# Kernel optimization log

Hardware: AMD Instinct MI355X
Metric: run time of the kernel (lower is better)

Reference implementation:

```python
import jax, jax.numpy as jnp
import numpy as np

B, N, NFEAT, NHID, NHEADS, NBLK = 8, 512, 32, 128, 4, 6


def _lrelu(x):
    return jax.nn.leaky_relu(x, 0.01)


def _layernorm(x, eps=1e-5):
    m = jnp.mean(x, axis=-1, keepdims=True)
    v = jnp.mean((x - m) ** 2, axis=-1, keepdims=True)
    return (x - m) / jnp.sqrt(v + eps)


def _gat(x, W, a, mask, concat):
    # x:[b,n,f]  W:[H,f,o]  a:[H,2o]  mask:[b,n,n] bool
    o = W.shape[-1]
    Wh = jnp.einsum('bnf,hfo->hbno', x, W)
    s1 = jnp.einsum('hbno,ho->hbn', Wh, a[:, :o])   # Wh @ a[:o]
    s2 = jnp.einsum('hbno,ho->hbn', Wh, a[:, o:])   # Wh @ a[o:]
    # rank-1 score: e[i,j] = leakyrelu(s1[i]*s2[j])
    e = _lrelu(s1[:, :, :, None] * s2[:, :, None, :])  # [h,b,n,n]
    e = jnp.where(mask[None], e, jnp.float32(-9e15))
    att = jax.nn.softmax(e, axis=-1)
    att = jnp.where(mask[None], att, jnp.float32(0.0))
    hp = jnp.einsum('hbij,hbjo->hbio', att, Wh)
    return jax.nn.elu(hp) if concat else hp


def _attn_block(x, W, a, rW, rb, mask):
    res = x
    h = _gat(x, W, a, mask, True)                      # [H,b,n,o]
    h = jnp.moveaxis(h, 0, 2).reshape(x.shape[0], x.shape[1], -1)  # concat heads
    h = h @ rW + rb
    if h.shape[-1] == res.shape[-1]:
        h = h + res
    return _layernorm(h)


def _fel(x, f1w1, f1b1, f1w2, f1b2, f2w1, f2b1, f2w2, f2b2, f3w1, f3b1, f3w2, f3b2):
    res = _lrelu(_lrelu(x @ f1w1 + f1b1) @ f1w2 + f1b2)
    h = _lrelu(_lrelu(res @ f2w1 + f2b1) @ f2w2 + f2b2)
    x = _layernorm(h + res)
    res = x
    h = _lrelu(res @ f3w1 + f3b1) @ f3w2 + f3b2
    return _layernorm(h + res)


def setup_inputs() -> dict:
    key = jax.random.key(0)
    ks = iter(jax.random.split(key, 24))
    nrm = lambda shape: jax.random.normal(next(ks), shape, jnp.float32) * 0.05
    inp = {}
    inp['x'] = jax.random.normal(next(ks), (B, N, NFEAT), jnp.float32)
    inp['adj'] = jax.random.randint(next(ks), (B, N, N), 0, 2, jnp.int32)
    inp['layer_id'] = 0
    inp['f1w1'] = nrm((NFEAT, NHID)); inp['f1b1'] = jnp.zeros((NHID,), jnp.float32)
    inp['f1w2'] = nrm((NHID, NHID)); inp['f1b2'] = jnp.zeros((NHID,), jnp.float32)
    inp['f2w1'] = nrm((NHID, 2 * NHID)); inp['f2b1'] = jnp.zeros((2 * NHID,), jnp.float32)
    inp['f2w2'] = nrm((2 * NHID, NHID)); inp['f2b2'] = jnp.zeros((NHID,), jnp.float32)
    inp['f3w1'] = nrm((NHID, 2 * NHID)); inp['f3b1'] = jnp.zeros((2 * NHID,), jnp.float32)
    inp['f3w2'] = nrm((2 * NHID, NHID)); inp['f3b2'] = jnp.zeros((NHID,), jnp.float32)
    inp['att_W'] = nrm((NBLK, NHEADS, NHID, NHID))
    inp['att_a'] = nrm((NBLK, NHEADS, 2 * NHID))
    inp['resh_W'] = nrm((NBLK, NHEADS * NHID, NHID))
    inp['resh_b'] = jnp.zeros((NBLK, NHID), jnp.float32)
    inp['out_W'] = nrm((2, NHID, NHID))
    inp['out_a'] = nrm((2, 2 * NHID))
    inp['proj_W'] = nrm((2 * NHID, 1))
    inp['proj_b'] = jnp.zeros((1,), jnp.float32)
    return inp


def reference(x, adj, layer_id, f1w1, f1b1, f1w2, f1b2, f2w1, f2b1, f2w2, f2b2,
              f3w1, f3b1, f3w2, f3b2, att_W, att_a, resh_W, resh_b, out_W, out_a,
              proj_W, proj_b):
    mask = adj > 0
    mask_t = jnp.transpose(adj, (0, 2, 1)) > 0
    h = _fel(x, f1w1, f1b1, f1w2, f1b2, f2w1, f2b1, f2w2, f2b2, f3w1, f3b1, f3w2, f3b2)
    for i in range(3):
        h = _attn_block(h, att_W[i], att_a[i], resh_W[i], resh_b[i], mask)
    h = _lrelu(_gat(h, out_W[0:1], out_a[0:1], mask, False)[0])
    ht = h
    for i in range(3, 6):
        ht = _attn_block(ht, att_W[i], att_a[i], resh_W[i], resh_b[i], mask_t)
    ht = _lrelu(_gat(ht, out_W[1:2], out_a[1:2], mask_t, False)[0])
    z = jnp.concatenate([h, ht], axis=-1)   # [b,n,2*nhid]
    z = jnp.mean(z, axis=1)                 # sum/length
    return jnp.squeeze(z @ proj_W + proj_b, axis=1)
```

## Files before the change

kernel.cpp:

```cpp
#include <hip/hip_runtime.h>
#include <math.h>

#define B 8
#define N 512
#define D 128
#define H 4
#define TOK (B*N)

typedef __attribute__((ext_vector_type(8))) short bfrag;
typedef __attribute__((ext_vector_type(4))) float facc;
typedef unsigned short u16;
typedef unsigned int u32;
typedef unsigned long long u64;

__device__ __forceinline__ float lrelu(float x){ return x > 0.f ? x : 0.01f*x; }
__device__ __forceinline__ u16 f2bf(float f){
  u32 u = __float_as_uint(f);
  u += 0x7fffu + ((u >> 16) & 1u);
  return (u16)(u >> 16);
}
__device__ __forceinline__ u32 pk2(float a, float b){
  return (u32)f2bf(a) | ((u32)f2bf(b) << 16);
}

#define LS 72
#define ASF 264
#define ASW 136

__global__ void prep_kernel(const int* __restrict__ adj,
    u32* __restrict__ mbits, u32* __restrict__ mtbits,
    float* __restrict__ colsumF, float* __restrict__ colsumT,
    const float* s0, const float* s1_, const float* s2_, const float* s3,
    const float* s4, const float* s5, const float* s6, const float* s7,
    const float* s8,
    u16* d0, u16* d1, u16* d2, u16* d3, u16* d4, u16* d5, u16* d6, u16* d7, u16* d8)
{
  __shared__ int smem[64*65];
  const int tid = threadIdx.x;
  if (blockIdx.x < 512){
    const int tb = blockIdx.x;
    const int b = tb >> 6, i0 = ((tb >> 3) & 7)*64, j0 = (tb & 7)*64;
    #pragma unroll
    for (int i = 0; i < 4; ++i){
      const int r = i*16 + (tid >> 4);
      const int c = (tid & 15)*4;
      int4 v = *(const int4*)&adj[((size_t)b*N + i0 + r)*N + j0 + c];
      smem[r*65 + c]     = v.x; smem[r*65 + c + 1] = v.y;
      smem[r*65 + c + 2] = v.z; smem[r*65 + c + 3] = v.w;
    }
    __syncthreads();
    const int wv = tid >> 6, lane = tid & 63;
    #pragma unroll
    for (int q = 0; q < 16; ++q){
      const int r = wv*16 + q;
      u64 bf_ = __ballot(smem[r*65 + lane] > 0);
      if (lane == 0)
        *(u64*)&mbits[((size_t)b*N + i0 + r)*16 + (j0 >> 5)] = bf_;
      u64 bt_ = __ballot(smem[lane*65 + r] > 0);
      if (lane == 0)
        *(u64*)&mtbits[((size_t)b*N + j0 + r)*16 + (i0 >> 5)] = bt_;
    }
  } else if (blockIdx.x < 1460){
    float* ftile = (float*)smem;
    const int tx = tid & 31, ty = tid >> 5;
    const float* srcs[9] = {s0,s1_,s2_,s3,s4,s5,s6,s7,s8};
    u16* dsts[9] = {d0,d1,d2,d3,d4,d5,d6,d7,d8};
    const int Ks[9] = {32,128,128,256,128,256,128,128,512};
    const int Ns[9] = {128,128,256,128,256,128,128,128,128};
    const int zs[9] = {1,1,1,1,1,1,24,2,6};
    const int job = (int)blockIdx.x - 512;
    int m = 0, base = 0;
    for (; m < 9; ++m){
      int cnt = (Ks[m]>>5)*(Ns[m]>>5)*zs[m];
      if (job < base + cnt) break;
      base += cnt;
    }
    const int rem = job - base;
    const int tn = Ns[m] >> 5;
    const int per = (Ks[m] >> 5)*tn;
    const int z = rem / per, t = rem % per;
    const int k0 = (t / tn)*32, n0 = (t % tn)*32;
    const float* src = srcs[m] + (size_t)z*Ks[m]*Ns[m];
    u16* dst = dsts[m] + (size_t)z*Ks[m]*Ns[m];
    for (int r = ty; r < 32; r += 8)
      ftile[r*33 + tx] = src[(size_t)(k0+r)*Ns[m] + n0 + tx];
    __syncthreads();
    for (int r = ty; r < 32; r += 8)
      dst[(size_t)(n0+r)*Ks[m] + k0 + tx] = f2bf(ftile[tx*33 + r]);
  } else {
    float4 z = {0.f,0.f,0.f,0.f};
    *(float4*)&colsumF[tid*4] = z;
    *(float4*)&colsumT[tid*4] = z;
  }
}

struct BPre { uint4 a,b,c,d; };
__device__ __forceinline__ BPre preB64(const u16* __restrict__ BTn, int ldb, int k0, int tid){
  const int n = tid >> 1, part = tid & 1;
  const u16* wp = BTn + (size_t)n*ldb + k0 + part*32;
  BPre r;
  r.a = *(const uint4*)wp;      r.b = *(const uint4*)(wp+8);
  r.c = *(const uint4*)(wp+16); r.d = *(const uint4*)(wp+24);
  return r;
}
__device__ __forceinline__ void landB64(const BPre& p, u16* Bs, int tid){
  const int n = tid >> 1, part = tid & 1;
  u16* bp = &Bs[n*LS + part*32];
  *(uint4*)bp = p.a; *(uint4*)(bp+8) = p.b; *(uint4*)(bp+16) = p.c; *(uint4*)(bp+24) = p.d;
}
__device__ __forceinline__ void stageB32(const u16* __restrict__ BTn, int ldb,
                                         int k0, u16* Bs, int tid){
  const int n = tid >> 1, part = tid & 1;
  const u16* wp = BTn + (size_t)n*ldb + k0 + part*16;
  uint4 w0 = *(const uint4*)wp, w1 = *(const uint4*)(wp+8);
  *(uint4*)&Bs[n*LS + part*16]     = w0;
  *(uint4*)&Bs[n*LS + part*16 + 8] = w1;
}

__device__ __forceinline__ void mfma64s(const u16* As, int sA, const u16* Bs,
                                        facc acc[4], int r0, int c0, int quad, int l15){
  #pragma unroll
  for (int kk = 0; kk < 2; ++kk){
    bfrag af = *(const bfrag*)&As[(r0 + l15)*sA + kk*32 + quad*8];
    #pragma unroll
    for (int g = 0; g < 4; ++g){
      bfrag bf = *(const bfrag*)&Bs[(c0 + g*16 + l15)*LS + kk*32 + quad*8];
      acc[g] = __builtin_amdgcn_mfma_f32_16x16x32_bf16(af, bf, acc[g], 0,0,0);
    }
  }
}
__device__ __forceinline__ void mfma32s(const u16* As, int sA, const u16* Bs,
                                        facc acc[4], int r0, int c0, int quad, int l15){
  bfrag af = *(const bfrag*)&As[(r0 + l15)*sA + quad*8];
  #pragma unroll
  for (int g = 0; g < 4; ++g){
    bfrag bf = *(const bfrag*)&Bs[(c0 + g*16 + l15)*LS + quad*8];
    acc[g] = __builtin_amdgcn_mfma_f32_16x16x32_bf16(af, bf, acc[g], 0,0,0);
  }
}
__device__ __forceinline__ void mfma64w(const u16* As, const u16* Bs,
                                        facc acc[2][2], int c0,
                                        int quad, int l15){
  #pragma unroll
  for (int kk = 0; kk < 2; ++kk){
    bfrag af0 = *(const bfrag*)&As[(l15)*LS      + kk*32 + quad*8];
    bfrag af1 = *(const bfrag*)&As[(16 + l15)*LS + kk*32 + quad*8];
    #pragma unroll
    for (int f = 0; f < 2; ++f){
      bfrag bf = *(const bfrag*)&Bs[(c0 + f*16 + l15)*LS + kk*32 + quad*8];
      acc[0][f] = __builtin_amdgcn_mfma_f32_16x16x32_bf16(af0, bf, acc[0][f], 0,0,0);
      acc[1][f] = __builtin_amdgcn_mfma_f32_16x16x32_bf16(af1, bf, acc[1][f], 0,0,0);
    }
  }
}

template<int T>
__device__ __forceinline__ void gemmAs(const u16* Aw, int sA,
    const u16* __restrict__ BT, int ldb, u16* Bs,
    facc acc[4], int tid, int r0, int c0, int quad, int l15){
  BPre p = preB64(BT, ldb, 0, tid);
  #pragma unroll
  for (int t = 0; t < T; ++t){
    __syncthreads();
    landB64(p, Bs, tid);
    if (t + 1 < T) p = preB64(BT, ldb, (t+1)*64, tid);
    __syncthreads();
    mfma64s(Aw + t*64, sA, Bs, acc, r0, c0, quad, l15);
  }
}

template<int NH>
__device__ __forceinline__ void wh_phaseS(const u16* Aw, int sA, u16* Bs,
    const u16* __restrict__ WT, const float* __restrict__ aatt,
    int t0, u16* __restrict__ WhT, float* __restrict__ s1, float* __restrict__ s2,
    float (*r1s4)[2][32], float (*r2s4)[2][32], int tid)
{
  const int wave = tid >> 6, lane = tid & 63, quad = lane >> 4, l15 = lane & 15;
  const int r0 = (wave & 1)*16, c0 = (wave >> 1)*64;
  const int b = t0 >> 9, j0 = t0 & (N-1);
  BPre p = preB64(WT, D, 0, tid);
  facc acc[4];
  #pragma unroll
  for (int t = 0; t < 2*NH; ++t){
    if ((t & 1) == 0){
      #pragma unroll
      for (int g = 0; g < 4; ++g) acc[g] = (facc){0.f,0.f,0.f,0.f};
    }
    __syncthreads();
    landB64(p, Bs, tid);
    if (t + 1 < 2*NH) p = preB64(WT + (size_t)((t+1)>>1)*D*D, D, ((t+1)&1)*64, tid);
    __syncthreads();
    mfma64s(Aw + (t&1)*64, sA, Bs, acc, r0, c0, quad, l15);
    if (t & 1){
      const int h = t >> 1;
      const float* ah = aatt + (size_t)h*2*D;
      const size_t obase = (size_t)(h*8 + b)*128;
      float p1[4] = {0,0,0,0}, p2[4] = {0,0,0,0};
      #pragma unroll
      for (int g = 0; g < 4; ++g){
        const int c = c0 + g*16 + l15;
        const float a1v = ah[c], a2v = ah[D + c];
        ushort4 wv;
        wv.x = f2bf(acc[g][0]); wv.y = f2bf(acc[g][1]);
        wv.z = f2bf(acc[g][2]); wv.w = f2bf(acc[g][3]);
        *(ushort4*)&WhT[(obase + c)*N + j0 + r0 + quad*4] = wv;
        #pragma unroll
        for (int q = 0; q < 4; ++q){
          p1[q] = fmaf(acc[g][q], a1v, p1[q]);
          p2[q] = fmaf(acc[g][q], a2v, p2[q]);
        }
      }
      #pragma unroll
      for (int m = 1; m < 16; m <<= 1){
        #pragma unroll
        for (int q = 0; q < 4; ++q){ p1[q] += __shfl_xor(p1[q], m, 64); p2[q] += __shfl_xor(p2[q], m, 64); }
      }
      if (l15 == 0){
        #pragma unroll
        for (int q = 0; q < 4; ++q){
          r1s4[h][wave>>1][r0 + quad*4 + q] = p1[q];
          r2s4[h][wave>>1][r0 + quad*4 + q] = p2[q];
        }
      }
    }
  }
  __syncthreads();
  if (tid < 32*NH){
    const int h = tid >> 5, r = tid & 31;
    s1[(size_t)h*TOK + t0 + r] = r1s4[h][0][r] + r1s4[h][1][r];
    s2[(size_t)h*TOK + t0 + r] = r2s4[h][0][r] + r2s4[h][1][r];
  }
}

__global__ __launch_bounds__(256) void fel_kernel(
    const float* __restrict__ x,
    const u16* __restrict__ w1T, const float* __restrict__ b1,
    const u16* __restrict__ w2T, const float* __restrict__ b2,
    const u16* __restrict__ w3T, const float* __restrict__ b3,
    const u16* __restrict__ w4T, const float* __restrict__ b4,
    const u16* __restrict__ w5T, const float* __restrict__ b5,
    const u16* __restrict__ w6T, const float* __restrict__ b6,
    const u16* __restrict__ WTatt, const float* __restrict__ aatt,
    float* __restrict__ hout, u16* __restrict__ WhT,
    float* __restrict__ s1, float* __restrict__ s2)
{
  const int tid = threadIdx.x;
  const int t0 = blockIdx.x * 32;
  __shared__ __align__(16) u16 AwA[32*ASF];
  __shared__ __align__(16) u16 AwB[32*ASF];
  __shared__ __align__(16) u16 Bs[128*LS];
  __shared__ float scrS[4][16], scrQ[4][16];
  __shared__ float r1s4[H][2][32], r2s4[H][2][32];
  const int wave = tid >> 6, lane = tid & 63, quad = lane >> 4, l15 = lane & 15;
  const int r0 = (wave & 1)*16, c0 = (wave >> 1)*64;
  facc acc[4];
  float rres[4][4];

  { const int row = tid >> 3, ko = tid & 7;
    float4 a0 = *(const float4*)(x + (size_t)(t0+row)*32 + ko*4);
    uint2 u = { pk2(a0.x,a0.y), pk2(a0.z,a0.w) };
    *(uint2*)&AwA[row*ASF + ko*4] = u;
    stageB32(w1T, 32, 0, Bs, tid);
  }
  __syncthreads();
  #pragma unroll
  for (int g = 0; g < 4; ++g) acc[g] = (facc){0.f,0.f,0.f,0.f};
  mfma32s(AwA, ASF, Bs, acc, r0, c0, quad, l15);
  #pragma unroll
  for (int g = 0; g < 4; ++g){
    const int c = c0 + g*16 + l15;
    const float bv = b1[c];
    #pragma unroll
    for (int q = 0; q < 4; ++q)
      AwB[(r0 + quad*4 + q)*ASF + c] = f2bf(lrelu(acc[g][q] + bv));
  }

  #pragma unroll
  for (int g = 0; g < 4; ++g) acc[g] = (facc){0.f,0.f,0.f,0.f};
  gemmAs<2>(AwB, ASF, w2T, 128, Bs, acc, tid, r0, c0, quad, l15);
  #pragma unroll
  for (int g = 0; g < 4; ++g){
    const int c = c0 + g*16 + l15;
    const float bv = b2[c];
    #pragma unroll
    for (int q = 0; q < 4; ++q){
      float xv = lrelu(acc[g][q] + bv);
      AwA[(r0 + quad*4 + q)*ASF + c] = f2bf(xv);
      rres[g][q] = xv;
    }
  }

  #pragma unroll
  for (int ch = 0; ch < 2; ++ch){
    #pragma unroll
    for (int g = 0; g < 4; ++g) acc[g] = (facc){0.f,0.f,0.f,0.f};
    gemmAs<2>(AwA, ASF, w3T + (size_t)ch*128*128, 128, Bs, acc, tid, r0, c0, quad, l15);
    #pragma unroll
    for (int g = 0; g < 4; ++g){
      const int c = c0 + g*16 + l15;
      const float bv = b3[ch*128 + c];
      #pragma unroll
      for (int q = 0; q < 4; ++q)
        AwB[(r0 + quad*4 + q)*ASF + ch*128 + c] = f2bf(lrelu(acc[g][q] + bv));
    }
  }

  #pragma unroll
  for (int g = 0; g < 4; ++g) acc[g] = (facc){0.f,0.f,0.f,0.f};
  gemmAs<4>(AwB, ASF, w4T, 256, Bs, acc, tid, r0, c0, quad, l15);
  {
    float v[4][4], s[4] = {0,0,0,0}, sq[4] = {0,0,0,0};
    #pragma unroll
    for (int g = 0; g < 4; ++g){
      const int c = c0 + g*16 + l15;
      const float bv = b4[c];
      #pragma unroll
      for (int q = 0; q < 4; ++q){
        float xv = lrelu(acc[g][q] + bv) + rres[g][q];
        v[g][q] = xv; s[q] += xv; sq[q] += xv*xv;
      }
    }
    #pragma unroll
    for (int m = 1; m < 16; m <<= 1){
      #pragma unroll
      for (int q = 0; q < 4; ++q){ s[q] += __shfl_xor(s[q], m, 64); sq[q] += __shfl_xor(sq[q], m, 64); }
    }
    if (l15 == 0){
      #pragma unroll
      for (int q = 0; q < 4; ++q){ scrS[wave][quad*4+q] = s[q]; scrQ[wave][quad*4+q] = sq[q]; }
    }
    __syncthreads();
    #pragma unroll
    for (int q = 0; q < 4; ++q){
      const int r = r0 + quad*4 + q;
      const float fs = s[q] + scrS[wave^2][quad*4+q];
      const float fq = sq[q] + scrQ[wave^2][quad*4+q];
      const float mean = fs*(1.f/D);
      const float rstd = rsqrtf(fq*(1.f/D) - mean*mean + 1e-5f);
      #pragma unroll
      for (int g = 0; g < 4; ++g){
        const int c = c0 + g*16 + l15;
        float xv = (v[g][q] - mean)*rstd;
        AwA[r*ASF + c] = f2bf(xv);
        rres[g][q] = xv;
      }
    }
  }

  #pragma unroll
  for (int ch = 0; ch < 2; ++ch){
    #pragma unroll
    for (int g = 0; g < 4; ++g) acc[g] = (facc){0.f,0.f,0.f,0.f};
    gemmAs<2>(AwA, ASF, w5T + (size_t)ch*128*128, 128, Bs, acc, tid, r0, c0, quad, l15);
    #pragma unroll
    for (int g = 0; g < 4; ++g){
      const int c = c0 + g*16 + l15;
      const float bv = b5[ch*128 + c];
      #pragma unroll
      for (int q = 0; q < 4; ++q)
        AwB[(r0 + quad*4 + q)*ASF + ch*128 + c] = f2bf(lrelu(acc[g][q] + bv));
    }
  }

  #pragma unroll
  for (int g = 0; g < 4; ++g) acc[g] = (facc){0.f,0.f,0.f,0.f};
  gemmAs<4>(AwB, ASF, w6T, 256, Bs, acc, tid, r0, c0, quad, l15);
  {
    float v[4][4], s[4] = {0,0,0,0}, sq[4] = {0,0,0,0};
    #pragma unroll
    for (int g = 0; g < 4; ++g){
      const int c = c0 + g*16 + l15;
      const float bv = b6[c];
      #pragma unroll
      for (int q = 0; q < 4; ++q){
        float xv = acc[g][q] + bv + rres[g][q];
        v[g][q] = xv; s[q] += xv; sq[q] += xv*xv;
      }
    }
    #pragma unroll
    for (int m = 1; m < 16; m <<= 1){
      #pragma unroll
      for (int q = 0; q < 4; ++q){ s[q] += __shfl_xor(s[q], m, 64); sq[q] += __shfl_xor(sq[q], m, 64); }
    }
    if (l15 == 0){
      #pragma unroll
      for (int q = 0; q < 4; ++q){ scrS[wave][quad*4+q] = s[q]; scrQ[wave][quad*4+q] = sq[q]; }
    }
    __syncthreads();
    #pragma unroll
    for (int q = 0; q < 4; ++q){
      const int r = r0 + quad*4 + q;
      const float fs = s[q] + scrS[wave^2][quad*4+q];
      const float fq = sq[q] + scrQ[wave^2][quad*4+q];
      const float mean = fs*(1.f/D);
      const float rstd = rsqrtf(fq*(1.f/D) - mean*mean + 1e-5f);
      #pragma unroll
      for (int g = 0; g < 4; ++g){
        const int c = c0 + g*16 + l15;
        float xv = (v[g][q] - mean)*rstd;
        hout[(size_t)(t0 + r)*128 + c] = xv;
        AwA[r*ASF + c] = f2bf(xv);
      }
    }
  }
  wh_phaseS<H>(AwA, ASF, Bs, WTatt, aatt, t0, WhT, s1, s2, r1s4, r2s4, tid);
}

template<int NH>
__global__ __launch_bounds__(256) void reshwh(
    const u16* __restrict__ A, const u16* __restrict__ BT, const float* __restrict__ bias,
    const float* __restrict__ res, float* __restrict__ hout,
    const u16* __restrict__ WT, const float* __restrict__ aatt,
    u16* __restrict__ WhT, float* __restrict__ s1, float* __restrict__ s2)
{
  const int tid = threadIdx.x;
  const int t0 = blockIdx.x * 32;
  __shared__ __align__(16) u16 AsU[2][32*LS];
  __shared__ __align__(16) u16 Bs[2][128*LS];
  __shared__ float scrS[4][32], scrQ[4][32];
  __shared__ float r1s4[NH][2][32], r2s4[NH][2][32];
  const int wave = tid >> 6, lane = tid & 63, quad = lane >> 4, l15 = lane & 15;
  const int c0w = wave*32;
  facc acc[2][2];
  #pragma unroll
  for (int rg = 0; rg < 2; ++rg)
    #pragma unroll
    for (int f = 0; f < 2; ++f) acc[rg][f] = (facc){0.f,0.f,0.f,0.f};

  const int arow = tid >> 3, ako = tid & 7;
  const u16* aptr = A + (size_t)(t0+arow)*512 + ako*8;
  const int bn = tid >> 1, bpart = tid & 1;
  const u16* bptr = BT + (size_t)bn*512 + bpart*32;

  { uint4 ga = *(const uint4*)aptr;
    uint4 g0 = *(const uint4*)bptr,      g1 = *(const uint4*)(bptr+8);
    uint4 g2 = *(const uint4*)(bptr+16), g3 = *(const uint4*)(bptr+24);
    *(uint4*)&AsU[0][arow*LS + ako*8] = ga;
    u16* bp = &Bs[0][bn*LS + bpart*32];
    *(uint4*)bp = g0; *(uint4*)(bp+8) = g1; *(uint4*)(bp+16) = g2; *(uint4*)(bp+24) = g3;
  }
  __syncthreads();
  #pragma unroll
  for (int k = 0; k < 7; ++k){
    const int cur = k & 1, nxt = cur ^ 1;
    uint4 na = *(const uint4*)(aptr + (k+1)*64);
    const u16* wp = bptr + (k+1)*64;
    uint4 n0 = *(const uint4*)wp,      n1 = *(const uint4*)(wp+8);
    uint4 n2 = *(const uint4*)(wp+16), n3 = *(const uint4*)(wp+24);
    mfma64w(AsU[cur], Bs[cur], acc, c0w, quad, l15);
    *(uint4*)&AsU[nxt][arow*LS + ako*8] = na;
    { u16* bp = &Bs[nxt][bn*LS + bpart*32];
      *(uint4*)bp = n0; *(uint4*)(bp+8) = n1; *(uint4*)(bp+16) = n2; *(uint4*)(bp+24) = n3; }
    __syncthreads();
  }
  mfma64w(AsU[1], Bs[1], acc, c0w, quad, l15);

  float bv[2];
  #pragma unroll
  for (int f = 0; f < 2; ++f) bv[f] = bias[c0w + f*16 + l15];
  float v[2][2][4], s[2][4], sq[2][4];
  #pragma unroll
  for (int rg = 0; rg < 2; ++rg)
    #pragma unroll
    for (int q = 0; q < 4; ++q){ s[rg][q] = 0.f; sq[rg][q] = 0.f; }
  #pragma unroll
  for (int rg = 0; rg < 2; ++rg){
    #pragma unroll
    for (int f = 0; f < 2; ++f){
      const int c = c0w + f*16 + l15;
      #pragma unroll
      for (int q = 0; q < 4; ++q){
        const int rq = t0 + rg*16 + quad*4 + q;
        float xv = acc[rg][f][q] + bv[f] + res[(size_t)rq*128 + c];
        v[rg][f][q] = xv; s[rg][q] += xv; sq[rg][q] += xv*xv;
      }
    }
  }
  #pragma unroll
  for (int m = 1; m < 16; m <<= 1){
    #pragma unroll
    for (int rg = 0; rg < 2; ++rg)
      #pragma unroll
      for (int q = 0; q < 4; ++q){ s[rg][q] += __shfl_xor(s[rg][q], m, 64); sq[rg][q] += __shfl_xor(sq[rg][q], m, 64); }
  }
  if (l15 == 0){
    #pragma unroll
    for (int rg = 0; rg < 2; ++rg)
      #pragma unroll
      for (int q = 0; q < 4; ++q){
        scrS[wave][rg*16 + quad*4 + q] = s[rg][q];
        scrQ[wave][rg*16 + quad*4 + q] = sq[rg][q];
      }
  }
  __syncthreads();
  u16* Aw = &AsU[0][0];
  #pragma unroll
  for (int rg = 0; rg < 2; ++rg){
    #pragma unroll
    for (int q = 0; q < 4; ++q){
      const int row = rg*16 + quad*4 + q;
      const float fs = scrS[0][row] + scrS[1][row] + scrS[2][row] + scrS[3][row];
      const float fq = scrQ[0][row] + scrQ[1][row] + scrQ[2][row] + scrQ[3][row];
      const float mean = fs*(1.f/D);
      const float rstd = rsqrtf(fq*(1.f/D) - mean*mean + 1e-5f);
      #pragma unroll
      for (int f = 0; f < 2; ++f){
        const int c = c0w + f*16 + l15;
        float xv = (v[rg][f][q] - mean)*rstd;
        hout[(size_t)(t0+row)*128 + c] = xv;
        Aw[row*ASW + c] = f2bf(xv);
      }
    }
  }
  wh_phaseS<NH>(Aw, ASW, &Bs[0][0], WT, aatt, t0, WhT, s1, s2, r1s4, r2s4, tid);
}

__device__ __forceinline__ float score8(const float* s2s, const unsigned char* mrow,
                                        float s1lr, int k0, int lq, u16* asp){
  float4 sa = *(const float4*)&s2s[k0 + lq*8];
  float4 sb = *(const float4*)&s2s[k0 + lq*8 + 4];
  const u32 mm = mrow[(k0 >> 3) + lq];
  float ss[8] = {sa.x,sa.y,sa.z,sa.w,sb.x,sb.y,sb.z,sb.w};
  float v[8]; float p = 0.f;
  #pragma unroll
  for (int i = 0; i < 8; ++i){
    float e = lrelu(s1lr * ss[i]);
    float ex = ((mm >> i) & 1u) ? __expf(e) : 0.f;
    v[i] = ex; p += ex;
  }
  uint4 u = { pk2(v[0],v[1]), pk2(v[2],v[3]), pk2(v[4],v[5]), pk2(v[6],v[7]) };
  *(uint4*)asp = u;
  return p;
}

__global__ __launch_bounds__(256) void pv32(
    const float* __restrict__ s1, const float* __restrict__ s2,
    const u32* __restrict__ mbits, const u16* __restrict__ WhT,
    u16* __restrict__ out_)
{
  const int tid = threadIdx.x;
  const int h  = blockIdx.x >> 7;
  const int t0 = (blockIdx.x & 127) * 32;
  const int b = t0 >> 9, i0 = t0 & (N-1);
  __shared__ float s2s[N];
  __shared__ float s1s[32], sums[32];
  __shared__ u32 mbs[32*16];
  __shared__ __align__(16) u16 As[2][32*LS];
  __shared__ __align__(16) u16 Bs[2][128*LS];

  s2s[tid]     = s2[(size_t)h*TOK + b*N + tid];
  s2s[tid+256] = s2[(size_t)h*TOK + b*N + tid + 256];
  if (tid < 32) s1s[tid] = s1[(size_t)h*TOK + t0 + tid];
  { const int r = tid >> 3, wd = (tid & 7)*2;
    *(uint2*)&mbs[r*16 + wd] = *(const uint2*)&mbits[((size_t)b*N + i0 + r)*16 + wd];
  }

  const u16* BTn = WhT + (size_t)(h*8 + b)*128*N;
  const int wave = tid >> 6, lane = tid & 63, quad = lane >> 4, l15 = lane & 15;
  const int c0 = wave*32;
  facc acc[2][2];
  #pragma unroll
  for (int rg = 0; rg < 2; ++rg)
    #pragma unroll
    for (int f = 0; f < 2; ++f) acc[rg][f] = (facc){0.f,0.f,0.f,0.f};

  const int lr = tid >> 3, lq = tid & 7;
  const unsigned char* mrow = (const unsigned char*)&mbs[lr*16];
  const int bn = tid >> 1, bpart = tid & 1;
  const u16* bwp = BTn + (size_t)bn*N + bpart*32;
  float psum = 0.f;

  uint4 g0 = *(const uint4*)bwp,      g1 = *(const uint4*)(bwp+8);
  uint4 g2 = *(const uint4*)(bwp+16), g3 = *(const uint4*)(bwp+24);
  __syncthreads();
  const float s1lr = s1s[lr];
  psum += score8(s2s, mrow, s1lr, 0, lq, &As[0][lr*LS + lq*8]);
  { u16* bp = &Bs[0][bn*LS + bpart*32];
    *(uint4*)bp = g0; *(uint4*)(bp+8) = g1; *(uint4*)(bp+16) = g2; *(uint4*)(bp+24) = g3; }
  __syncthreads();

  #pragma unroll
  for (int k = 0; k < 7; ++k){
    const int cur = k & 1, nxt = cur ^ 1;
    const u16* wp = bwp + (k+1)*64;
    uint4 n0 = *(const uint4*)wp,      n1 = *(const uint4*)(wp+8);
    uint4 n2 = *(const uint4*)(wp+16), n3 = *(const uint4*)(wp+24);
    psum += score8(s2s, mrow, s1lr, (k+1)*64, lq, &As[nxt][lr*LS + lq*8]);
    mfma64w(As[cur], Bs[cur], acc, c0, quad, l15);
    { u16* bp = &Bs[nxt][bn*LS + bpart*32];
      *(uint4*)bp = n0; *(uint4*)(bp+8) = n1; *(uint4*)(bp+16) = n2; *(uint4*)(bp+24) = n3; }
    __syncthreads();
  }
  mfma64w(As[1], Bs[1], acc, c0, quad, l15);

  #pragma unroll
  for (int m = 1; m < 8; m <<= 1) psum += __shfl_xor(psum, m, 64);
  if (lq == 0) sums[lr] = psum;
  __syncthreads();

  #pragma unroll
  for (int rg = 0; rg < 2; ++rg){
    #pragma unroll
    for (int q = 0; q < 4; ++q){
      const int row = rg*16 + quad*4 + q;
      const float sv = sums[row];
      const float inv = sv > 0.f ? 1.f/sv : 0.f;
      const int rq = t0 + row;
      #pragma unroll
      for (int f = 0; f < 2; ++f){
        float xv = acc[rg][f][q] * inv;
        xv = xv > 0.f ? xv : __expf(xv) - 1.f;
        out_[(size_t)rq*512 + h*128 + c0 + f*16 + l15] = f2bf(xv);
      }
    }
  }
}

template<int DOWH>
__global__ __launch_bounds__(256) void pvout(
    const float* __restrict__ s1in, const float* __restrict__ s2in,
    const u32* __restrict__ mbits, const u16* __restrict__ WhTin,
    float* __restrict__ hF, float* __restrict__ colsum,
    const u16* __restrict__ WT, const float* __restrict__ aatt,
    u16* __restrict__ WhTout, float* __restrict__ s1out, float* __restrict__ s2out)
{
  const int tid = threadIdx.x;
  const int t0 = blockIdx.x * 32;
  const int b = t0 >> 9, i0 = t0 & (N-1);
  __shared__ float s2s[N];
  __shared__ float s1s[32], sums[32];
  __shared__ u32 mbs[32*16];
  __shared__ __align__(16) u16 AsU[2][32*LS];
  __shared__ __align__(16) u16 Bs[2][128*LS];
  __shared__ float r1s4[H][2][32], r2s4[H][2][32];

  s2s[tid]     = s2in[b*N + tid];
  s2s[tid+256] = s2in[b*N + tid + 256];
  if (tid < 32) s1s[tid] = s1in[t0 + tid];
  { const int r = tid >> 3, wd = (tid & 7)*2;
    *(uint2*)&mbs[r*16 + wd] = *(const uint2*)&mbits[((size_t)b*N + i0 + r)*16 + wd];
  }

  const u16* BTn = WhTin + (size_t)b*128*N;
  const int wave = tid >> 6, lane = tid & 63, quad = lane >> 4, l15 = lane & 15;
  const int c0w = wave*32;
  facc acc[2][2];
  #pragma unroll
  for (int rg = 0; rg < 2; ++rg)
    #pragma unroll
    for (int f = 0; f < 2; ++f) acc[rg][f] = (facc){0.f,0.f,0.f,0.f};

  const int lr = tid >> 3, lq = tid & 7;
  const unsigned char* mrow = (const unsigned char*)&mbs[lr*16];
  const int bn = tid >> 1, bpart = tid & 1;
  const u16* bwp = BTn + (size_t)bn*N + bpart*32;
  float psum = 0.f;

  uint4 g0 = *(const uint4*)bwp,      g1 = *(const uint4*)(bwp+8);
  uint4 g2 = *(const uint4*)(bwp+16), g3 = *(const uint4*)(bwp+24);
  __syncthreads();
  const float s1lr = s1s[lr];
  psum += score8(s2s, mrow, s1lr, 0, lq, &AsU[0][lr*LS + lq*8]);
  { u16* bp = &Bs[0][bn*LS + bpart*32];
    *(uint4*)bp = g0; *(uint4*)(bp+8) = g1; *(uint4*)(bp+16) = g2; *(uint4*)(bp+24) = g3; }
  __syncthreads();

  #pragma unroll
  for (int k = 0; k < 7; ++k){
    const int cur = k & 1, nxt = cur ^ 1;
    const u16* wp = bwp + (k+1)*64;
    uint4 n0 = *(const uint4*)wp,      n1 = *(const uint4*)(wp+8);
    uint4 n2 = *(const uint4*)(wp+16), n3 = *(const uint4*)(wp+24);
    psum += score8(s2s, mrow, s1lr, (k+1)*64, lq, &AsU[nxt][lr*LS + lq*8]);
    mfma64w(AsU[cur], Bs[cur], acc, c0w, quad, l15);
    { u16* bp = &Bs[nxt][bn*LS + bpart*32];
      *(uint4*)bp = n0; *(uint4*)(bp+8) = n1; *(uint4*)(bp+16) = n2; *(uint4*)(bp+24) = n3; }
    __syncthreads();
  }
  mfma64w(AsU[1], Bs[1], acc, c0w, quad, l15);

  #pragma unroll
  for (int m = 1; m < 8; m <<= 1) psum += __shfl_xor(psum, m, 64);
  if (lq == 0) sums[lr] = psum;
  __syncthreads();

  u16* Aw = &AsU[0][0];
  float pcs[2] = {0.f, 0.f};
  #pragma unroll
  for (int rg = 0; rg < 2; ++rg){
    #pragma unroll
    for (int q = 0; q < 4; ++q){
      const int row = rg*16 + quad*4 + q;
      const float sv = sums[row];
      const float inv = sv > 0.f ? 1.f/sv : 0.f;
      #pragma unroll
      for (int f = 0; f < 2; ++f){
        const int c = c0w + f*16 + l15;
        float xv = lrelu(acc[rg][f][q] * inv);
        if (DOWH){
          hF[(size_t)(t0+row)*128 + c] = xv;
          Aw[row*ASW + c] = f2bf(xv);
        }
        pcs[f] += xv;
      }
    }
  }
  pcs[0] += __shfl_xor(pcs[0], 16, 64); pcs[0] += __shfl_xor(pcs[0], 32, 64);
  pcs[1] += __shfl_xor(pcs[1], 16, 64); pcs[1] += __shfl_xor(pcs[1], 32, 64);
  if (quad == 0){
    atomicAdd(&colsum[b*128 + c0w + l15], pcs[0]);
    atomicAdd(&colsum[b*128 + c0w + 16 + l15], pcs[1]);
  }
  if (DOWH)
    wh_phaseS<H>(Aw, ASW, &Bs[0][0], WT, aatt, t0, WhTout, s1out, s2out, r1s4, r2s4, tid);
}

__global__ void final_kernel(const float* __restrict__ colsumF, const float* __restrict__ colsumT,
                             const float* __restrict__ pW, const float* __restrict__ pb,
                             float* __restrict__ out)
{
  const int b = blockIdx.x, c = threadIdx.x;
  __shared__ float scr[4];
  float s = ((c < D) ? colsumF[b*D + c] : colsumT[b*D + (c - D)]) * (1.f/N);
  float p = s * pW[c];
  #pragma unroll
  for (int m = 32; m; m >>= 1) p += __shfl_xor(p, m, 64);
  if ((c & 63) == 0) scr[c >> 6] = p;
  __syncthreads();
  if (c == 0) out[b] = scr[0] + scr[1] + scr[2] + scr[3] + pb[0];
}

extern "C" void kernel_launch(void* const* d_in, const int* in_sizes, int n_in,
                              void* d_out, int out_size, void* d_ws, size_t ws_size,
                              hipStream_t stream)
{
  (void)in_sizes; (void)n_in; (void)out_size; (void)ws_size;
  const float* x    = (const float*)d_in[0];
  const int*   adj  = (const int*)d_in[1];
  const float* f1w1 = (const float*)d_in[3];
  const float* f1b1 = (const float*)d_in[4];
  const float* f1w2 = (const float*)d_in[5];
  const float* f1b2 = (const float*)d_in[6];
  const float* f2w1 = (const float*)d_in[7];
  const float* f2b1 = (const float*)d_in[8];
  const float* f2w2 = (const float*)d_in[9];
  const float* f2b2 = (const float*)d_in[10];
  const float* f3w1 = (const float*)d_in[11];
  const float* f3b1 = (const float*)d_in[12];
  const float* f3w2 = (const float*)d_in[13];
  const float* f3b2 = (const float*)d_in[14];
  const float* attW = (const float*)d_in[15];
  const float* attA = (const float*)d_in[16];
  const float* rshW = (const float*)d_in[17];
  const float* rshB = (const float*)d_in[18];
  const float* outW = (const float*)d_in[19];
  const float* outA = (const float*)d_in[20];
  const float* pW   = (const float*)d_in[21];
  const float* pb   = (const float*)d_in[22];

  char* w = (char*)d_ws;
  float* hA  = (float*)w; w += (size_t)TOK*128*4;
  float* hB  = (float*)w; w += (size_t)TOK*128*4;
  float* hF  = (float*)w; w += (size_t)TOK*128*4;
  u16*  hp2  = (u16*)w;  w += (size_t)TOK*512*2;
  u16*  WhT  = (u16*)w;  w += (size_t)H*8*128*N*2;
  u16*  WhT2 = (u16*)w;  w += (size_t)H*8*128*N*2;
  float* s1  = (float*)w; w += (size_t)H*TOK*4;
  float* s2  = (float*)w; w += (size_t)H*TOK*4;
  float* s1b = (float*)w; w += (size_t)H*TOK*4;
  float* s2b = (float*)w; w += (size_t)H*TOK*4;
  u32* mbits = (u32*)w;  w += (size_t)B*N*16*4;
  u32* mtbits= (u32*)w;  w += (size_t)B*N*16*4;
  float* colsumF = (float*)w; w += (size_t)B*128*4;
  float* colsumT = (float*)w; w += (size_t)B*128*4;
  u16* f1w1T = (u16*)w; w += 128*32*2;
  u16* f1w2T = (u16*)w; w += 128*128*2;
  u16* f2w1T = (u16*)w; w += 256*128*2;
  u16* f2w2T = (u16*)w; w += 128*256*2;
  u16* f3w1T = (u16*)w; w += 256*128*2;
  u16* f3w2T = (u16*)w; w += 128*256*2;
  u16* attWT = (u16*)w; w += (size_t)24*128*128*2;
  u16* outWT = (u16*)w; w += (size_t)2*128*128*2;
  u16* rshWT = (u16*)w; w += (size_t)6*128*512*2;

  prep_kernel<<<1461,256,0,stream>>>(adj, mbits, mtbits, colsumF, colsumT,
      f1w1, f1w2, f2w1, f2w2, f3w1, f3w2, attW, outW, rshW,
      f1w1T, f1w2T, f2w1T, f2w2T, f3w1T, f3w2T, attWT, outWT, rshWT);

  fel_kernel<<<128,256,0,stream>>>(x,
      f1w1T, f1b1, f1w2T, f1b2, f2w1T, f2b1, f2w2T, f2b2, f3w1T, f3b1, f3w2T, f3b2,
      attWT, attA, hA, WhT, s1, s2);

  pv32<<<H*128,256,0,stream>>>(s1, s2, mbits, WhT, hp2);
  reshwh<4><<<128,256,0,stream>>>(hp2, rshWT + 0*128*512, rshB + 0*D, hA, hB,
      attWT + (size_t)1*H*D*D, attA + (size_t)1*H*2*D, WhT, s1, s2);
  pv32<<<H*128,256,0,stream>>>(s1, s2, mbits, WhT, hp2);
  reshwh<4><<<128,256,0,stream>>>(hp2, rshWT + (size_t)1*128*512, rshB + 1*D, hB, hA,
      attWT + (size_t)2*H*D*D, attA + (size_t)2*H*2*D, WhT, s1, s2);
  pv32<<<H*128,256,0,stream>>>(s1, s2, mbits, WhT, hp2);
  reshwh<1><<<128,256,0,stream>>>(hp2, rshWT + (size_t)2*128*512, rshB + 2*D, hA, hB,
      outWT, outA, WhT, s1, s2);

  pvout<1><<<128,256,0,stream>>>(s1, s2, mbits, WhT, hF, colsumF,
      attWT + (size_t)3*H*D*D, attA + (size_t)3*H*2*D, WhT2, s1b, s2b);

  pv32<<<H*128,256,0,stream>>>(s1b, s2b, mtbits, WhT2, hp2);
  reshwh<4><<<128,256,0,stream>>>(hp2, rshWT + (size_t)3*128*512, rshB + 3*D, hF, hA,
      attWT + (size_t)4*H*D*D, attA + (size_t)4*H*2*D, WhT, s1, s2);
  pv32<<<H*128,256,0,stream>>>(s1, s2, mtbits, WhT, hp2);
  reshwh<4><<<128,256,0,stream>>>(hp2, rshWT + (size_t)4*128*512, rshB + 4*D, hA, hB,
      attWT + (size_t)5*H*D*D, attA + (size_t)5*H*2*D, WhT, s1, s2);
  pv32<<<H*128,256,0,stream>>>(s1, s2, mtbits, WhT, hp2);
  reshwh<1><<<128,256,0,stream>>>(hp2, rshWT + (size_t)5*128*512, rshB + 5*D, hB, hA,
      outWT + 128*128, outA + 2*D, WhT, s1, s2);

  pvout<0><<<128,256,0,stream>>>(s1, s2, mtbits, WhT, nullptr, colsumT,
      nullptr, nullptr, nullptr, nullptr, nullptr);

  final_kernel<<<B,2*D,0,stream>>>(colsumF, colsumT, pW, pb, (float*)d_out);
}
```

Before: 307.5 us.

## Double threads per block in pv32 and reshwh, splitting output columns across two groups

```diff
diff --git a/kernel.cpp b/kernel.cpp
--- a/kernel.cpp
+++ b/kernel.cpp
@@ -116,6 +116,17 @@
   *(uint4*)&Bs[n*LS + part*16]     = w0;
   *(uint4*)&Bs[n*LS + part*16 + 8] = w1;
 }
+struct BPre2 { uint4 a,b; };
+__device__ __forceinline__ BPre2 preBh(const u16* __restrict__ BTn, int ldb, int k0,
+                                       int gtid, int rowoff){
+  const u16* wp = BTn + (size_t)(rowoff + (gtid >> 2))*ldb + k0 + (gtid & 3)*16;
+  BPre2 r; r.a = *(const uint4*)wp; r.b = *(const uint4*)(wp+8);
+  return r;
+}
+__device__ __forceinline__ void landBh(const BPre2& p, u16* Bs, int gtid){
+  u16* bp = &Bs[(gtid >> 2)*LS + (gtid & 3)*16];
+  *(uint4*)bp = p.a; *(uint4*)(bp+8) = p.b;
+}
 
 __device__ __forceinline__ void mfma64s(const u16* As, int sA, const u16* Bs,
                                         facc acc[4], int r0, int c0, int quad, int l15){
@@ -151,6 +162,17 @@
       acc[0][f] = __builtin_amdgcn_mfma_f32_16x16x32_bf16(af0, bf, acc[0][f], 0,0,0);
       acc[1][f] = __builtin_amdgcn_mfma_f32_16x16x32_bf16(af1, bf, acc[1][f], 0,0,0);
     }
+  }
+}
+__device__ __forceinline__ void mfma64h(const u16* As, const u16* Bs,
+                                        facc acc[2], int c0, int quad, int l15){
+  #pragma unroll
+  for (int kk = 0; kk < 2; ++kk){
+    bfrag af0 = *(const bfrag*)&As[(l15)*LS      + kk*32 + quad*8];
+    bfrag af1 = *(const bfrag*)&As[(16 + l15)*LS + kk*32 + quad*8];
+    bfrag bf  = *(const bfrag*)&Bs[(c0 + l15)*LS + kk*32 + quad*8];
+    acc[0] = __builtin_amdgcn_mfma_f32_16x16x32_bf16(af0, bf, acc[0], 0,0,0);
+    acc[1] = __builtin_amdgcn_mfma_f32_16x16x32_bf16(af1, bf, acc[1], 0,0,0);
   }
 }
 
@@ -407,7 +429,7 @@
 }
 
 template<int NH>
-__global__ __launch_bounds__(256) void reshwh(
+__global__ __launch_bounds__(512) void reshwh(
     const u16* __restrict__ A, const u16* __restrict__ BT, const float* __restrict__ bias,
     const float* __restrict__ res, float* __restrict__ hout,
     const u16* __restrict__ WT, const float* __restrict__ aatt,
@@ -416,80 +438,62 @@
   const int tid = threadIdx.x;
   const int t0 = blockIdx.x * 32;
   __shared__ __align__(16) u16 AsU[2][32*LS];
-  __shared__ __align__(16) u16 Bs[2][128*LS];
-  __shared__ float scrS[4][32], scrQ[4][32];
+  __shared__ __align__(16) u16 Bsg[2][2][64*LS];
+  __shared__ float scrS[8][32], scrQ[8][32];
   __shared__ float r1s4[NH][2][32], r2s4[NH][2][32];
-  const int wave = tid >> 6, lane = tid & 63, quad = lane >> 4, l15 = lane & 15;
-  const int c0w = wave*32;
-  facc acc[2][2];
-  #pragma unroll
-  for (int rg = 0; rg < 2; ++rg)
-    #pragma unroll
-    for (int f = 0; f < 2; ++f) acc[rg][f] = (facc){0.f,0.f,0.f,0.f};
-
-  const int arow = tid >> 3, ako = tid & 7;
-  const u16* aptr = A + (size_t)(t0+arow)*512 + ako*8;
-  const int bn = tid >> 1, bpart = tid & 1;
-  const u16* bptr = BT + (size_t)bn*512 + bpart*32;
-
-  { uint4 ga = *(const uint4*)aptr;
-    uint4 g0 = *(const uint4*)bptr,      g1 = *(const uint4*)(bptr+8);
-    uint4 g2 = *(const uint4*)(bptr+16), g3 = *(const uint4*)(bptr+24);
-    *(uint4*)&AsU[0][arow*LS + ako*8] = ga;
-    u16* bp = &Bs[0][bn*LS + bpart*32];
-    *(uint4*)bp = g0; *(uint4*)(bp+8) = g1; *(uint4*)(bp+16) = g2; *(uint4*)(bp+24) = g3;
+  const int g = tid >> 8, gtid = tid & 255;
+  const int w8 = tid >> 6, lane = tid & 63, quad = lane >> 4, l15 = lane & 15;
+  const int wv = gtid >> 6;
+  const int c0h = wv*16;
+
+  facc acc2[2];
+  acc2[0] = (facc){0.f,0.f,0.f,0.f}; acc2[1] = (facc){0.f,0.f,0.f,0.f};
+  const int arow = tid >> 4, ako = tid & 15;
+  const u16* aptr = A + (size_t)(t0+arow)*512 + ako*4;
+  { uint2 a0 = *(const uint2*)aptr;
+    BPre2 b0 = preBh(BT, 512, 0, gtid, g*64);
+    *(uint2*)&AsU[0][arow*LS + ako*4] = a0;
+    landBh(b0, Bsg[g][0], gtid);
   }
   __syncthreads();
   #pragma unroll
   for (int k = 0; k < 7; ++k){
     const int cur = k & 1, nxt = cur ^ 1;
-    uint4 na = *(const uint4*)(aptr + (k+1)*64);
-    const u16* wp = bptr + (k+1)*64;
-    uint4 n0 = *(const uint4*)wp,      n1 = *(const uint4*)(wp+8);
-    uint4 n2 = *(const uint4*)(wp+16), n3 = *(const uint4*)(wp+24);
-    mfma64w(AsU[cur], Bs[cur], acc, c0w, quad, l15);
-    *(uint4*)&AsU[nxt][arow*LS + ako*8] = na;
-    { u16* bp = &Bs[nxt][bn*LS + bpart*32];
-      *(uint4*)bp = n0; *(uint4*)(bp+8) = n1; *(uint4*)(bp+16) = n2; *(uint4*)(bp+24) = n3; }
-    __syncthreads();
-  }
-  mfma64w(AsU[1], Bs[1], acc, c0w, quad, l15);
-
-  float bv[2];
-  #pragma unroll
-  for (int f = 0; f < 2; ++f) bv[f] = bias[c0w + f*16 + l15];
-  float v[2][2][4], s[2][4], sq[2][4];
-  #pragma unroll
-  for (int rg = 0; rg < 2; ++rg)
-    #pragma unroll
-    for (int q = 0; q < 4; ++q){ s[rg][q] = 0.f; sq[rg][q] = 0.f; }
+    uint2 na = *(const uint2*)(aptr + (k+1)*64);
+    BPre2 nb = preBh(BT, 512, (k+1)*64, gtid, g*64);
+    mfma64h(AsU[cur], Bsg[g][cur], acc2, c0h, quad, l15);
+    *(uint2*)&AsU[nxt][arow*LS + ako*4] = na;
+    landBh(nb, Bsg[g][nxt], gtid);
+    __syncthreads();
+  }
+  mfma64h(AsU[1], Bsg[g][1], acc2, c0h, quad, l15);
+
+  const int c = g*64 + c0h + l15;
+  const float bv = bias[c];
+  float v[2][4], s[2][4], sq[2][4];
   #pragma unroll
   for (int rg = 0; rg < 2; ++rg){
     #pragma unroll
-    for (int f = 0; f < 2; ++f){
-      const int c = c0w + f*16 + l15;
+    for (int q = 0; q < 4; ++q){
+      const int rq = t0 + rg*16 + quad*4 + q;
+      float xv = acc2[rg][q] + bv + res[(size_t)rq*128 + c];
+      v[rg][q] = xv; s[rg][q] = xv; sq[rg][q] = xv*xv;
+    }
+  }
+  #pragma unroll
+  for (int m = 1; m < 16; m <<= 1){
+    #pragma unroll
+    for (int rg = 0; rg < 2; ++rg)
+      #pragma unroll
+      for (int q = 0; q < 4; ++q){ s[rg][q] += __shfl_xor(s[rg][q], m, 64); sq[rg][q] += __shfl_xor(sq[rg][q], m, 64); }
+  }
+  if (l15 == 0){
+    #pragma unroll
+    for (int rg = 0; rg < 2; ++rg)
       #pragma unroll
       for (int q = 0; q < 4; ++q){
-        const int rq = t0 + rg*16 + quad*4 + q;
-        float xv = acc[rg][f][q] + bv[f] + res[(size_t)rq*128 + c];
-        v[rg][f][q] = xv; s[rg][q] += xv; sq[rg][q] += xv*xv;
-      }
-    }
-  }
-  #pragma unroll
-  for (int m = 1; m < 16; m <<= 1){
-    #pragma unroll
-    for (int rg = 0; rg < 2; ++rg)
-      #pragma unroll
-      for (int q = 0; q < 4; ++q){ s[rg][q] += __shfl_xor(s[rg][q], m, 64); sq[rg][q] += __shfl_xor(sq[rg][q], m, 64); }
-  }
-  if (l15 == 0){
-    #pragma unroll
-    for (int rg = 0; rg < 2; ++rg)
-      #pragma unroll
-      for (int q = 0; q < 4; ++q){
-        scrS[wave][rg*16 + quad*4 + q] = s[rg][q];
-        scrQ[wave][rg*16 + quad*4 + q] = sq[rg][q];
+        scrS[w8][rg*16 + quad*4 + q] = s[rg][q];
+        scrQ[w8][rg*16 + quad*4 + q] = sq[rg][q];
       }
   }
   __syncthreads();
@@ -499,22 +503,99 @@
     #pragma unroll
     for (int q = 0; q < 4; ++q){
       const int row = rg*16 + quad*4 + q;
-      const float fs = scrS[0][row] + scrS[1][row] + scrS[2][row] + scrS[3][row];
-      const float fq = scrQ[0][row] + scrQ[1][row] + scrQ[2][row] + scrQ[3][row];
+      float fs = 0.f, fq = 0.f;
+      #pragma unroll
+      for (int w = 0; w < 8; ++w){ fs += scrS[w][row]; fq += scrQ[w][row]; }
       const float mean = fs*(1.f/D);
       const float rstd = rsqrtf(fq*(1.f/D) - mean*mean + 1e-5f);
-      #pragma unroll
-      for (int f = 0; f < 2; ++f){
-        const int c = c0w + f*16 + l15;
-        float xv = (v[rg][f][q] - mean)*rstd;
-        hout[(size_t)(t0+row)*128 + c] = xv;
-        Aw[row*ASW + c] = f2bf(xv);
-      }
-    }
-  }
-  wh_phaseS<NH>(Aw, ASW, &Bs[0][0], WT, aatt, t0, WhT, s1, s2, r1s4, r2s4, tid);
-}
-
+      float xv = (v[rg][q] - mean)*rstd;
+      hout[(size_t)(t0+row)*128 + c] = xv;
+      Aw[row*ASW + c] = f2bf(xv);
+    }
+  }
+  __syncthreads();
+
+  const int NHg = (NH == 4) ? 2 : 1;
+  const int hbase = (NH == 4) ? g*2 : 0;
+  const bool st = (NH == 4) || (g == 0);
+  u16* BsW = &Bsg[g][0][0];
+  const int r0w = (wv & 1)*16, c0w = (wv >> 1)*64;
+  const int b = t0 >> 9, j0 = t0 & (N-1);
+  facc acc[4];
+  BPre p = preB64(WT + (size_t)hbase*D*D, D, 0, gtid);
+  #pragma unroll
+  for (int t = 0; t < 2*NHg; ++t){
+    if ((t & 1) == 0){
+      #pragma unroll
+      for (int gg = 0; gg < 4; ++gg) acc[gg] = (facc){0.f,0.f,0.f,0.f};
+    }
+    __syncthreads();
+    landB64(p, BsW, gtid);
+    if (t + 1 < 2*NHg){
+      const int hn = hbase + ((t+1) >> 1);
+      p = preB64(WT + (size_t)hn*D*D, D, ((t+1)&1)*64, gtid);
+    }
+    __syncthreads();
+    mfma64s(Aw + (t&1)*64, ASW, BsW, acc, r0w, c0w, quad, l15);
+    if (t & 1){
+      const int h = hbase + (t >> 1);
+      const float* ah = aatt + (size_t)h*2*D;
+      const size_t obase = (size_t)(h*8 + b)*128;
+      float p1[4] = {0,0,0,0}, p2[4] = {0,0,0,0};
+      #pragma unroll
+      for (int gg = 0; gg < 4; ++gg){
+        const int cc = c0w + gg*16 + l15;
+        const float a1v = ah[cc], a2v = ah[D + cc];
+        if (st){
+          ushort4 wvv;
+          wvv.x = f2bf(acc[gg][0]); wvv.y = f2bf(acc[gg][1]);
+          wvv.z = f2bf(acc[gg][2]); wvv.w = f2bf(acc[gg][3]);
+          *(ushort4*)&WhT[(obase + cc)*N + j0 + r0w + quad*4] = wvv;
+        }
+        #pragma unroll
+        for (int q = 0; q < 4; ++q){
+          p1[q] = fmaf(acc[gg][q], a1v, p1[q]);
+          p2[q] = fmaf(acc[gg][q], a2v, p2[q]);
+        }
+      }
+      #pragma unroll
+      for (int m = 1; m < 16; m <<= 1){
+        #pragma unroll
+        for (int q = 0; q < 4; ++q){ p1[q] += __shfl_xor(p1[q], m, 64); p2[q] += __shfl_xor(p2[q], m, 64); }
+      }
+      if (st && l15 == 0){
+        #pragma unroll
+        for (int q = 0; q < 4; ++q){
+          r1s4[h][wv>>1][r0w + quad*4 + q] = p1[q];
+          r2s4[h][wv>>1][r0w + quad*4 + q] = p2[q];
+        }
+      }
+    }
+  }
+  __syncthreads();
+  if (tid < 32*NH){
+    const int h = tid >> 5, r = tid & 31;
+    s1[(size_t)h*TOK + t0 + r] = r1s4[h][0][r] + r1s4[h][1][r];
+    s2[(size_t)h*TOK + t0 + r] = r2s4[h][0][r] + r2s4[h][1][r];
+  }
+}
+
+__device__ __forceinline__ float score4(const float* s2s, const unsigned char* mrow,
+                                        float s1lr, int k0, int ls, u16* asp){
+  float4 sa = *(const float4*)&s2s[k0 + ls*4];
+  const u32 mm = (u32)(mrow[(k0 >> 3) + (ls >> 1)]) >> ((ls & 1)*4);
+  float ss[4] = {sa.x,sa.y,sa.z,sa.w};
+  float v[4]; float p = 0.f;
+  #pragma unroll
+  for (int i = 0; i < 4; ++i){
+    float e = lrelu(s1lr * ss[i]);
+    float ex = ((mm >> i) & 1u) ? __expf(e) : 0.f;
+    v[i] = ex; p += ex;
+  }
+  uint2 u = { pk2(v[0],v[1]), pk2(v[2],v[3]) };
+  *(uint2*)asp = u;
+  return p;
+}
 __device__ __forceinline__ float score8(const float* s2s, const unsigned char* mrow,
                                         float s1lr, int k0, int lq, u16* asp){
   float4 sa = *(const float4*)&s2s[k0 + lq*8];
@@ -533,7 +614,7 @@
   return p;
 }
 
-__global__ __launch_bounds__(256) void pv32(
+__global__ __launch_bounds__(512) void pv32(
     const float* __restrict__ s1, const float* __restrict__ s2,
     const u32* __restrict__ mbits, const u16* __restrict__ WhT,
     u16* __restrict__ out_)
@@ -546,56 +627,46 @@
   __shared__ float s1s[32], sums[32];
   __shared__ u32 mbs[32*16];
   __shared__ __align__(16) u16 As[2][32*LS];
-  __shared__ __align__(16) u16 Bs[2][128*LS];
-
-  s2s[tid]     = s2[(size_t)h*TOK + b*N + tid];
-  s2s[tid+256] = s2[(size_t)h*TOK + b*N + tid + 256];
+  __shared__ __align__(16) u16 Bs[2][2][64*LS];
+
+  const int g = tid >> 8, gtid = tid & 255;
+  const int lane = tid & 63, quad = lane >> 4, l15 = lane & 15;
+  const int wv = gtid >> 6;
+  const int c0h = wv*16;
+
+  s2s[tid] = s2[(size_t)h*TOK + b*N + tid];
   if (tid < 32) s1s[tid] = s1[(size_t)h*TOK + t0 + tid];
-  { const int r = tid >> 3, wd = (tid & 7)*2;
-    *(uint2*)&mbs[r*16 + wd] = *(const uint2*)&mbits[((size_t)b*N + i0 + r)*16 + wd];
-  }
+  mbs[tid] = mbits[((size_t)b*N + i0 + (tid >> 4))*16 + (tid & 15)];
 
   const u16* BTn = WhT + (size_t)(h*8 + b)*128*N;
-  const int wave = tid >> 6, lane = tid & 63, quad = lane >> 4, l15 = lane & 15;
-  const int c0 = wave*32;
-  facc acc[2][2];
-  #pragma unroll
-  for (int rg = 0; rg < 2; ++rg)
-    #pragma unroll
-    for (int f = 0; f < 2; ++f) acc[rg][f] = (facc){0.f,0.f,0.f,0.f};
-
-  const int lr = tid >> 3, lq = tid & 7;
+  facc acc2[2];
+  acc2[0] = (facc){0.f,0.f,0.f,0.f}; acc2[1] = (facc){0.f,0.f,0.f,0.f};
+
+  const int lr = tid >> 4, ls = tid & 15;
   const unsigned char* mrow = (const unsigned char*)&mbs[lr*16];
-  const int bn = tid >> 1, bpart = tid & 1;
-  const u16* bwp = BTn + (size_t)bn*N + bpart*32;
   float psum = 0.f;
 
-  uint4 g0 = *(const uint4*)bwp,      g1 = *(const uint4*)(bwp+8);
-  uint4 g2 = *(const uint4*)(bwp+16), g3 = *(const uint4*)(bwp+24);
+  BPre2 p0 = preBh(BTn, N, 0, gtid, g*64);
   __syncthreads();
   const float s1lr = s1s[lr];
-  psum += score8(s2s, mrow, s1lr, 0, lq, &As[0][lr*LS + lq*8]);
-  { u16* bp = &Bs[0][bn*LS + bpart*32];
-    *(uint4*)bp = g0; *(uint4*)(bp+8) = g1; *(uint4*)(bp+16) = g2; *(uint4*)(bp+24) = g3; }
+  psum += score4(s2s, mrow, s1lr, 0, ls, &As[0][lr*LS + ls*4]);
+  landBh(p0, Bs[g][0], gtid);
   __syncthreads();
 
   #pragma unroll
   for (int k = 0; k < 7; ++k){
     const int cur = k & 1, nxt = cur ^ 1;
-    const u16* wp = bwp + (k+1)*64;
-    uint4 n0 = *(const uint4*)wp,      n1 = *(const uint4*)(wp+8);
-    uint4 n2 = *(const uint4*)(wp+16), n3 = *(const uint4*)(wp+24);
-    psum += score8(s2s, mrow, s1lr, (k+1)*64, lq, &As[nxt][lr*LS + lq*8]);
-    mfma64w(As[cur], Bs[cur], acc, c0, quad, l15);
-    { u16* bp = &Bs[nxt][bn*LS + bpart*32];
-      *(uint4*)bp = n0; *(uint4*)(bp+8) = n1; *(uint4*)(bp+16) = n2; *(uint4*)(bp+24) = n3; }
-    __syncthreads();
-  }
-  mfma64w(As[1], Bs[1], acc, c0, quad, l15);
-
-  #pragma unroll
-  for (int m = 1; m < 8; m <<= 1) psum += __shfl_xor(psum, m, 64);
-  if (lq == 0) sums[lr] = psum;
+    BPre2 np = preBh(BTn, N, (k+1)*64, gtid, g*64);
+    psum += score4(s2s, mrow, s1lr, (k+1)*64, ls, &As[nxt][lr*LS + ls*4]);
+    mfma64h(As[cur], Bs[g][cur], acc2, c0h, quad, l15);
+    landBh(np, Bs[g][nxt], gtid);
+    __syncthreads();
+  }
+  mfma64h(As[1], Bs[g][1], acc2, c0h, quad, l15);
+
+  #pragma unroll
+  for (int m = 1; m < 16; m <<= 1) psum += __shfl_xor(psum, m, 64);
+  if (ls == 0) sums[lr] = psum;
   __syncthreads();
 
   #pragma unroll
@@ -605,13 +676,9 @@
       const int row = rg*16 + quad*4 + q;
       const float sv = sums[row];
       const float inv = sv > 0.f ? 1.f/sv : 0.f;
-      const int rq = t0 + row;
-      #pragma unroll
-      for (int f = 0; f < 2; ++f){
-        float xv = acc[rg][f][q] * inv;
-        xv = xv > 0.f ? xv : __expf(xv) - 1.f;
-        out_[(size_t)rq*512 + h*128 + c0 + f*16 + l15] = f2bf(xv);
-      }
+      float xv = acc2[rg][q] * inv;
+      xv = xv > 0.f ? xv : __expf(xv) - 1.f;
+      out_[(size_t)(t0+row)*512 + h*128 + g*64 + c0h + l15] = f2bf(xv);
     }
   }
 }
@@ -791,27 +858,27 @@
       f1w1T, f1b1, f1w2T, f1b2, f2w1T, f2b1, f2w2T, f2b2, f3w1T, f3b1, f3w2T, f3b2,
       attWT, attA, hA, WhT, s1, s2);
 
-  pv32<<<H*128,256,0,stream>>>(s1, s2, mbits, WhT, hp2);
-  reshwh<4><<<128,256,0,stream>>>(hp2, rshWT + 0*128*512, rshB + 0*D, hA, hB,
+  pv32<<<H*128,512,0,stream>>>(s1, s2, mbits, WhT, hp2);
+  reshwh<4><<<128,512,0,stream>>>(hp2, rshWT + 0*128*512, rshB + 0*D, hA, hB,
       attWT + (size_t)1*H*D*D, attA + (size_t)1*H*2*D, WhT, s1, s2);
-  pv32<<<H*128,256,0,stream>>>(s1, s2, mbits, WhT, hp2);
-  reshwh<4><<<128,256,0,stream>>>(hp2, rshWT + (size_t)1*128*512, rshB + 1*D, hB, hA,
+  pv32<<<H*128,512,0,stream>>>(s1, s2, mbits, WhT, hp2);
+  reshwh<4><<<128,512,0,stream>>>(hp2, rshWT + (size_t)1*128*512, rshB + 1*D, hB, hA,
       attWT + (size_t)2*H*D*D, attA + (size_t)2*H*2*D, WhT, s1, s2);
-  pv32<<<H*128,256,0,stream>>>(s1, s2, mbits, WhT, hp2);
-  reshwh<1><<<128,256,0,stream>>>(hp2, rshWT + (size_t)2*128*512, rshB + 2*D, hA, hB,
+  pv32<<<H*128,512,0,stream>>>(s1, s2, mbits, WhT, hp2);
+  reshwh<1><<<128,512,0,stream>>>(hp2, rshWT + (size_t)2*128*512, rshB + 2*D, hA, hB,
       outWT, outA, WhT, s1, s2);
 
   pvout<1><<<128,256,0,stream>>>(s1, s2, mbits, WhT, hF, colsumF,
       attWT + (size_t)3*H*D*D, attA + (size_t)3*H*2*D, WhT2, s1b, s2b);
 
-  pv32<<<H*128,256,0,stream>>>(s1b, s2b, mtbits, WhT2, hp2);
-  reshwh<4><<<128,256,0,stream>>>(hp2, rshWT + (size_t)3*128*512, rshB + 3*D, hF, hA,
+  pv32<<<H*128,512,0,stream>>>(s1b, s2b, mtbits, WhT2, hp2);
+  reshwh<4><<<128,512,0,stream>>>(hp2, rshWT + (size_t)3*128*512, rshB + 3*D, hF, hA,
       attWT + (size_t)4*H*D*D, attA + (size_t)4*H*2*D, WhT, s1, s2);
-  pv32<<<H*128,256,0,stream>>>(s1, s2, mtbits, WhT, hp2);
-  reshwh<4><<<128,256,0,stream>>>(hp2, rshWT + (size_t)4*128*512, rshB + 4*D, hA, hB,
+  pv32<<<H*128,512,0,stream>>>(s1, s2, mtbits, WhT, hp2);
+  reshwh<4><<<128,512,0,stream>>>(hp2, rshWT + (size_t)4*128*512, rshB + 4*D, hA, hB,
       attWT + (size_t)5*H*D*D, attA + (size_t)5*H*2*D, WhT, s1, s2);
-  pv32<<<H*128,256,0,stream>>>(s1, s2, mtbits, WhT, hp2);
-  reshwh<1><<<128,256,0,stream>>>(hp2, rshWT + (size_t)5*128*512, rshB + 5*D, hB, hA,
+  pv32<<<H*128,512,0,stream>>>(s1, s2, mtbits, WhT, hp2);
+  reshwh<1><<<128,512,0,stream>>>(hp2, rshWT + (size_t)5*128*512, rshB + 5*D, hB, hA,
       outWT + 128*128, outA + 2*D, WhT, s1, s2);
 
   pvout<0><<<128,256,0,stream>>>(s1, s2, mtbits, WhT, nullptr, colsumT,
```

Measured after the change: 303.8 us. Within noise of the previous version (-1.2%).
